# Optimization experiments

Hardware: AMD Instinct MI355X
Metric: run time of the kernel (lower is better)

The kernel has to match this reference:

```python
import jax, jax.numpy as jnp
import numpy as np

EMBED_DIM = 512
NUM_HEADS = 8
HEAD_DIM = EMBED_DIM // NUM_HEADS
SCALE = HEAD_DIM ** -0.5


def setup_inputs() -> dict:
    key = jax.random.key(0)
    k_x, k_qkv, k_o, k_ob = jax.random.split(key, 4)
    x = jax.random.normal(k_x, (2, 2048, EMBED_DIM), dtype=jnp.float32)
    # torch Linear weight is [out, in]; we store transposed [in, out] for x @ W
    w_qkv = jax.random.normal(k_qkv, (EMBED_DIM, 3 * EMBED_DIM), dtype=jnp.float32) * (EMBED_DIM ** -0.5)
    w_o = jax.random.normal(k_o, (EMBED_DIM, EMBED_DIM), dtype=jnp.float32) * (EMBED_DIM ** -0.5)
    b_o = jax.random.normal(k_ob, (EMBED_DIM,), dtype=jnp.float32) * 0.01
    return {"x": x, "w_qkv": w_qkv, "w_o": w_o, "b_o": b_o}


def reference(x, w_qkv, w_o, b_o):
    b, s, e = x.shape
    qkv = x @ w_qkv  # [b, s, 3e]
    q, k, v = jnp.split(qkv, 3, axis=-1)
    # [b, s, e] -> [b, h, s, d]
    def heads(t):
        return t.reshape(b, s, NUM_HEADS, HEAD_DIM).transpose(0, 2, 1, 3)
    q, k, v = heads(q), heads(k), heads(v)
    scores = jnp.einsum("bhqd,bhkd->bhqk", q, k) * SCALE
    attn = jax.nn.softmax(scores, axis=-1)  # dropout = identity in eval
    out = jnp.einsum("bhqk,bhkd->bhqd", attn, v)
    out = out.transpose(0, 2, 1, 3).reshape(b, s, e)
    return out @ w_o + b_o
```

## Files before the change

kernel.cpp:

```cpp
#include <hip/hip_runtime.h>
#include <stdint.h>


typedef __bf16 bf16x8 __attribute__((ext_vector_type(8)));
typedef __bf16 bf16x4 __attribute__((ext_vector_type(4)));
typedef float f32x4 __attribute__((ext_vector_type(4)));
typedef float f32x16 __attribute__((ext_vector_type(16)));

#define MFMA16(a, b, c) __builtin_amdgcn_mfma_f32_16x16x32_bf16((a), (b), (c), 0, 0, 0)
#define MFMA32(a, b, c) __builtin_amdgcn_mfma_f32_32x32x16_bf16((a), (b), (c), 0, 0, 0)
#define QSC 0.18033688011112042f

__device__ __forceinline__ unsigned short f2bf(float f) {
  union { float f; unsigned int u; } v;
  v.f = f;
  unsigned int u = v.u;
  u += 0x7fffu + ((u >> 16) & 1u);
  return (unsigned short)(u >> 16);
}

__device__ __forceinline__ float fast_exp2(float x) {
#if __has_builtin(__builtin_amdgcn_exp2f)
  return __builtin_amdgcn_exp2f(x);
#else
  return exp2f(x);
#endif
}

__device__ __forceinline__ unsigned cvtpk_bf16(float lo, float hi) {
  unsigned r;
  asm("v_cvt_pk_bf16_f32 %0, %1, %2" : "=v"(r) : "v"(lo), "v"(hi));
  return r;
}

__device__ __forceinline__ void gld16(const void* g, void* lds) {
  __builtin_amdgcn_global_load_lds(
      (const __attribute__((address_space(1))) unsigned int*)g,
      (__attribute__((address_space(3))) unsigned int*)lds, 16, 0, 0);
}

__global__ void cvt_kernel(const float* __restrict__ in, unsigned short* __restrict__ out, int n4) {
  int i = blockIdx.x * blockDim.x + threadIdx.x;
  if (i < n4) {
    float4 v = ((const float4*)in)[i];
    ushort4 o;
    o.x = f2bf(v.x); o.y = f2bf(v.y); o.z = f2bf(v.z); o.w = f2bf(v.w);
    ((ushort4*)out)[i] = o;
  }
}

__global__ void tcvt_kernel(const float* __restrict__ in, unsigned short* __restrict__ out, int N) {
  __shared__ unsigned short tile[32][33];
  int tx = threadIdx.x & 31, ty = threadIdx.x >> 5;
  int n0 = blockIdx.x * 32, k0 = blockIdx.y * 32;
#pragma unroll
  for (int i = 0; i < 4; ++i)
    tile[ty + i * 8][tx] = f2bf(in[(k0 + ty + i * 8) * N + n0 + tx]);
  __syncthreads();
#pragma unroll
  for (int i = 0; i < 4; ++i)
    out[(n0 + ty + i * 8) * 512 + k0 + tx] = tile[tx][ty + i * 8];
}

__global__ __launch_bounds__(256, 2) void gemm_qkv(
    const unsigned short* __restrict__ A, const unsigned short* __restrict__ Bt,
    unsigned short* __restrict__ qws, unsigned short* __restrict__ kws,
    unsigned short* __restrict__ vtws) {
  __shared__ __align__(16) unsigned short As[2][128 * 64];
  __shared__ __align__(16) unsigned short Bs[2][128 * 64];
  const int tid = threadIdx.x;
  const int wave = tid >> 6, lane = tid & 63;
  const int quad = lane >> 4, l16 = lane & 15;
  const int waveM = (wave & 1) * 64, waveN = (wave >> 1) * 64;
  const int bm = blockIdx.x, bn = blockIdx.y;

  f32x4 acc[4][4] = {};

  const unsigned short* Ab = A + bm * 128 * 512;
  const unsigned short* Bb = Bt + bn * 128 * 512;

  auto stage = [&](int buf, int k0) {
#pragma unroll
    for (int c = 0; c < 4; ++c) {
      int p = wave * 256 + c * 64 + lane;
      int row = p >> 3;
      int ccl = (p & 7) ^ (row & 7);
      gld16(Ab + row * 512 + k0 + ccl * 8, (char*)(As[buf]) + (wave * 256 + c * 64) * 16);
      gld16(Bb + row * 512 + k0 + ccl * 8, (char*)(Bs[buf]) + (wave * 256 + c * 64) * 16);
    }
  };

  stage(0, 0);
  int cur = 0;
  for (int k0 = 0; k0 < 512; k0 += 64) {
    __syncthreads();
    if (k0 + 64 < 512) stage(cur ^ 1, k0 + 64);
    const unsigned short* Asc = As[cur];
    const unsigned short* Bsc = Bs[cur];
#pragma unroll
    for (int ks = 0; ks < 2; ++ks) {
      bf16x8 af[4], bfr[4];
#pragma unroll
      for (int mb = 0; mb < 4; ++mb) {
        int m = waveM + mb * 16 + l16;
        int cc = (ks * 4 + quad) ^ (m & 7);
        af[mb] = *(const bf16x8*)(Asc + m * 64 + cc * 8);
      }
#pragma unroll
      for (int nb = 0; nb < 4; ++nb) {
        int n = waveN + nb * 16 + l16;
        int cc = (ks * 4 + quad) ^ (n & 7);
        bfr[nb] = *(const bf16x8*)(Bsc + n * 64 + cc * 8);
      }
#pragma unroll
      for (int mb = 0; mb < 4; ++mb)
#pragma unroll
        for (int nb = 0; nb < 4; ++nb)
          acc[mb][nb] = MFMA16(af[mb], bfr[nb], acc[mb][nb]);
    }
    cur ^= 1;
  }

  const int mbase = bm * 128 + waveM;
  const int nbase = bn * 128 + waveN;
  const int region = nbase >> 9;
#pragma unroll
  for (int mb = 0; mb < 4; ++mb) {
    int m0 = mbase + mb * 16 + quad * 4;
    int b = m0 >> 11, s0 = m0 & 2047;
#pragma unroll
    for (int nb = 0; nb < 4; ++nb) {
      int n = nbase + nb * 16 + l16;
      int cix = n & 511;
      int h = cix >> 6, d = cix & 63;
      int bh = b * 8 + h;
      if (region == 0) {
#pragma unroll
        for (int r = 0; r < 4; ++r)
          qws[(bh * 2048 + s0 + r) * 64 + d] = f2bf(acc[mb][nb][r] * QSC);
      } else if (region == 1) {
#pragma unroll
        for (int r = 0; r < 4; ++r)
          kws[(bh * 2048 + s0 + r) * 64 + d] = f2bf(acc[mb][nb][r]);
      } else {
        ushort4 pk;
        pk.x = f2bf(acc[mb][nb][0]);
        pk.y = f2bf(acc[mb][nb][1]);
        pk.z = f2bf(acc[mb][nb][2]);
        pk.w = f2bf(acc[mb][nb][3]);
        *(ushort4*)(vtws + (bh * 64 + d) * 2048 + s0) = pk;
      }
    }
  }
}

__global__ __launch_bounds__(256, 2) void attn_kernel(
    const unsigned short* __restrict__ qws, const unsigned short* __restrict__ kws,
    const unsigned short* __restrict__ vtws, __bf16* __restrict__ opart,
    float* __restrict__ lpart) {
  __shared__ __align__(16) unsigned short Ks[2][64 * 64];
  __shared__ __align__(16) unsigned short Vs[2][64 * 64];
  const int tid = threadIdx.x;
  const int wave = tid >> 6, lane = tid & 63;
  const int l31 = lane & 31, hi = lane >> 5, l7 = lane & 7;
  const int qb = blockIdx.x, bh = blockIdx.y, split = blockIdx.z;

  const unsigned short* Qb = qws + bh * 2048 * 64;
  const unsigned short* Kb = kws + bh * 2048 * 64;
  const unsigned short* Vb = vtws + bh * 64 * 2048;

  const int qbase = qb * 128 + wave * 32;

  bf16x8 qf[4];
#pragma unroll
  for (int kc = 0; kc < 4; ++kc)
    qf[kc] = *(const bf16x8*)(Qb + (qbase + l31) * 64 + kc * 16 + hi * 8);

  float l_lane = 0.f;
  f32x16 oacc[2] = {};

  const int kt0 = split * 16;

  auto stage = [&](int buf, int kt) {
#pragma unroll
    for (int c = 0; c < 2; ++c) {
      int p = wave * 128 + c * 64 + lane;
      int row = p >> 3;
      int ccl = (p & 7) ^ (row & 7);
      gld16(Kb + (kt * 64 + row) * 64 + ccl * 8, (char*)(Ks[buf]) + (wave * 128 + c * 64) * 16);
      gld16(Vb + row * 2048 + kt * 64 + ccl * 8, (char*)(Vs[buf]) + (wave * 128 + c * 64) * 16);
    }
  };

  stage(0, kt0);
  int cur = 0;
  for (int i = 0; i < 16; ++i) {
    __syncthreads();
    if (i + 1 < 16) stage(cur ^ 1, kt0 + i + 1);
    const unsigned short* Kst = Ks[cur];
    const unsigned short* Vst = Vs[cur];

    bf16x8 pa[4];
#pragma unroll
    for (int t = 0; t < 2; ++t) {
      f32x16 sacc = {};
      __builtin_amdgcn_s_setprio(1);
#pragma unroll
      for (int kc = 0; kc < 4; ++kc) {
        bf16x8 kf = *(const bf16x8*)(Kst + (t * 32 + l31) * 64 + (((kc * 2 + hi) ^ l7) * 8));
        sacc = MFMA32(kf, qf[kc], sacc);
      }
      __builtin_amdgcn_s_setprio(0);
      float p[16];
#pragma unroll
      for (int r = 0; r < 16; ++r) p[r] = fast_exp2(sacc[r]);
      float ls = 0.f;
#pragma unroll
      for (int r = 0; r < 16; r += 4) ls += ((p[r] + p[r + 1]) + (p[r + 2] + p[r + 3]));
      l_lane += ls;
#pragma unroll
      for (int kcl = 0; kcl < 2; ++kcl) {
        unsigned c0 = cvtpk_bf16(p[8 * kcl + 0], p[8 * kcl + 1]);
        unsigned c1 = cvtpk_bf16(p[8 * kcl + 2], p[8 * kcl + 3]);
        unsigned c2 = cvtpk_bf16(p[8 * kcl + 4], p[8 * kcl + 5]);
        unsigned c3 = cvtpk_bf16(p[8 * kcl + 6], p[8 * kcl + 7]);
        asm("v_permlane32_swap_b32 %0, %1" : "+v"(c0), "+v"(c2));
        asm("v_permlane32_swap_b32 %0, %1" : "+v"(c1), "+v"(c3));
        union { unsigned u[4]; bf16x8 v; } pk;
        pk.u[0] = c0; pk.u[1] = c1; pk.u[2] = c2; pk.u[3] = c3;
        pa[t * 2 + kcl] = pk.v;
      }
    }

    __builtin_amdgcn_s_setprio(1);
#pragma unroll
    for (int kc2 = 0; kc2 < 4; ++kc2) {
#pragma unroll
      for (int dh = 0; dh < 2; ++dh) {
        bf16x8 vf = *(const bf16x8*)(Vst + (dh * 32 + l31) * 64 + (((kc2 * 2 + hi) ^ l7) * 8));
        oacc[dh] = MFMA32(pa[kc2], vf, oacc[dh]);
      }
    }
    __builtin_amdgcn_s_setprio(0);
    cur ^= 1;
  }

  const long ob = (long)(split * 16 + bh) * 2048;
#pragma unroll
  for (int dh = 0; dh < 2; ++dh)
#pragma unroll
    for (int r = 0; r < 16; ++r) {
      int ql = (r & 3) + 8 * (r >> 2) + 4 * hi;
      opart[(ob + qbase + ql) * 64 + dh * 32 + l31] = (__bf16)oacc[dh][r];
    }
  l_lane += __shfl_xor(l_lane, 32);
  if (hi == 0) lpart[ob + qbase + l31] = l_lane;
}

__global__ void combine_kernel(const __bf16* __restrict__ opart, const float* __restrict__ lpart,
                               unsigned short* __restrict__ ows) {
  int idx = blockIdx.x * 256 + threadIdx.x;
  int dg = idx & 15;
  int q = (idx >> 4) & 2047;
  int bh = idx >> 15;
  bf16x4 o0 = *(const bf16x4*)(opart + ((long)bh * 2048 + q) * 64 + dg * 4);
  bf16x4 o1 = *(const bf16x4*)(opart + ((long)(16 + bh) * 2048 + q) * 64 + dg * 4);
  float inv = 1.0f / (lpart[bh * 2048 + q] + lpart[16 * 2048 + bh * 2048 + q]);
  bf16x4 o;
#pragma unroll
  for (int i = 0; i < 4; ++i) o[i] = (__bf16)(((float)o0[i] + (float)o1[i]) * inv);
  int b = bh >> 3, h = bh & 7;
  *(bf16x4*)((__bf16*)ows + ((long)(b * 2048 + q)) * 512 + h * 64 + dg * 4) = o;
}

__global__ __launch_bounds__(256, 2) void gemm_out(
    const unsigned short* __restrict__ A, const unsigned short* __restrict__ Bt,
    const float* __restrict__ bias, float* __restrict__ out) {
  __shared__ __align__(16) unsigned short As[2][128 * 64];
  __shared__ __align__(16) unsigned short Bs[2][128 * 64];
  const int tid = threadIdx.x;
  const int wave = tid >> 6, lane = tid & 63;
  const int quad = lane >> 4, l16 = lane & 15;
  const int waveM = (wave & 1) * 64, waveN = (wave >> 1) * 64;
  const int bm = blockIdx.x, bn = blockIdx.y;

  f32x4 acc[4][4] = {};

  const unsigned short* Ab = A + bm * 128 * 512;
  const unsigned short* Bb = Bt + bn * 128 * 512;

  auto stage = [&](int buf, int k0) {
#pragma unroll
    for (int c = 0; c < 4; ++c) {
      int p = wave * 256 + c * 64 + lane;
      int row = p >> 3;
      int ccl = (p & 7) ^ (row & 7);
      gld16(Ab + row * 512 + k0 + ccl * 8, (char*)(As[buf]) + (wave * 256 + c * 64) * 16);
      gld16(Bb + row * 512 + k0 + ccl * 8, (char*)(Bs[buf]) + (wave * 256 + c * 64) * 16);
    }
  };

  stage(0, 0);
  int cur = 0;
  for (int k0 = 0; k0 < 512; k0 += 64) {
    __syncthreads();
    if (k0 + 64 < 512) stage(cur ^ 1, k0 + 64);
    const unsigned short* Asc = As[cur];
    const unsigned short* Bsc = Bs[cur];
#pragma unroll
    for (int ks = 0; ks < 2; ++ks) {
      bf16x8 af[4], bfr[4];
#pragma unroll
      for (int mb = 0; mb < 4; ++mb) {
        int m = waveM + mb * 16 + l16;
        int cc = (ks * 4 + quad) ^ (m & 7);
        af[mb] = *(const bf16x8*)(Asc + m * 64 + cc * 8);
      }
#pragma unroll
      for (int nb = 0; nb < 4; ++nb) {
        int n = waveN + nb * 16 + l16;
        int cc = (ks * 4 + quad) ^ (n & 7);
        bfr[nb] = *(const bf16x8*)(Bsc + n * 64 + cc * 8);
      }
#pragma unroll
      for (int mb = 0; mb < 4; ++mb)
#pragma unroll
        for (int nb = 0; nb < 4; ++nb)
          acc[mb][nb] = MFMA16(af[mb], bfr[nb], acc[mb][nb]);
    }
    cur ^= 1;
  }

  const int mbase = bm * 128 + waveM;
  const int nbase = bn * 128 + waveN;
#pragma unroll
  for (int mb = 0; mb < 4; ++mb) {
#pragma unroll
    for (int nb = 0; nb < 4; ++nb) {
      int n = nbase + nb * 16 + l16;
      float bv = bias[n];
#pragma unroll
      for (int r = 0; r < 4; ++r) {
        int m = mbase + mb * 16 + quad * 4 + r;
        out[m * 512 + n] = acc[mb][nb][r] + bv;
      }
    }
  }
}

extern "C" void kernel_launch(void* const* d_in, const int* in_sizes, int n_in,
                              void* d_out, int out_size, void* d_ws, size_t ws_size,
                              hipStream_t stream) {
  const float* x = (const float*)d_in[0];
  const float* w_qkv = (const float*)d_in[1];
  const float* w_o = (const float*)d_in[2];
  const float* b_o = (const float*)d_in[3];
  float* out = (float*)d_out;

  char* ws = (char*)d_ws;
  unsigned short* woT   = (unsigned short*)(ws + 0);
  unsigned short* qws   = (unsigned short*)(ws + 524288);
  unsigned short* kws   = (unsigned short*)(ws + 4718592);
  unsigned short* vtws  = (unsigned short*)(ws + 8912896);
  unsigned short* ows   = (unsigned short*)(ws + 13107200);
  __bf16*         opart = (__bf16*)(ws + 17301504);
  unsigned short* xb    = (unsigned short*)(ws + 17301504);
  unsigned short* wqkvT = (unsigned short*)(ws + 21495808);
  float*          lpart = (float*)(ws + 25690112);

  cvt_kernel<<<2048, 256, 0, stream>>>(x, xb, 524288);
  tcvt_kernel<<<dim3(48, 16), 256, 0, stream>>>(w_qkv, wqkvT, 1536);
  tcvt_kernel<<<dim3(16, 16), 256, 0, stream>>>(w_o, woT, 512);
  gemm_qkv<<<dim3(32, 12), 256, 0, stream>>>(xb, wqkvT, qws, kws, vtws);
  attn_kernel<<<dim3(16, 16, 2), 256, 0, stream>>>(qws, kws, vtws, opart, lpart);
  combine_kernel<<<2048, 256, 0, stream>>>(opart, lpart, ows);
  gemm_out<<<dim3(32, 4), 256, 0, stream>>>(ows, woT, b_o, out);
}
```

Before: 126.6 us.

## Fuse split-KV combine into output GEMM A-staging and merge prep kernels

Merges the three conversion and transpose kernels into one prep kernel dispatched by block index, which saves two launches. Removes the separate combine kernel: the output projection GEMM now reads both attention partials and their softmax denominators, normalizes them, and writes the bf16 A tile straight into shared memory. The GEMM tile M is halved to 64, giving a 64x4 grid for more blocks. The cost is that A staging becomes synchronous register loads instead of async global-to-LDS copies, and the combine work is repeated for each of the 4 N-blocks.

Measured after the change: 120.0 us. 1.06x faster.

```diff
diff --git a/kernel.cpp b/kernel.cpp
--- a/kernel.cpp
+++ b/kernel.cpp
@@ -39,27 +39,33 @@
       (__attribute__((address_space(3))) unsigned int*)lds, 16, 0, 0);
 }
 
-__global__ void cvt_kernel(const float* __restrict__ in, unsigned short* __restrict__ out, int n4) {
-  int i = blockIdx.x * blockDim.x + threadIdx.x;
-  if (i < n4) {
-    float4 v = ((const float4*)in)[i];
+__global__ void prep_kernel(const float* __restrict__ x, unsigned short* __restrict__ xb,
+                            const float* __restrict__ w_qkv, unsigned short* __restrict__ wqkvT,
+                            const float* __restrict__ w_o, unsigned short* __restrict__ woT) {
+  __shared__ unsigned short tile[32][33];
+  const int bid = blockIdx.x, tid = threadIdx.x;
+  if (bid < 2048) {
+    int i = bid * 256 + tid;
+    float4 v = ((const float4*)x)[i];
     ushort4 o;
     o.x = f2bf(v.x); o.y = f2bf(v.y); o.z = f2bf(v.z); o.w = f2bf(v.w);
-    ((ushort4*)out)[i] = o;
-  }
-}
-
-__global__ void tcvt_kernel(const float* __restrict__ in, unsigned short* __restrict__ out, int N) {
-  __shared__ unsigned short tile[32][33];
-  int tx = threadIdx.x & 31, ty = threadIdx.x >> 5;
-  int n0 = blockIdx.x * 32, k0 = blockIdx.y * 32;
-#pragma unroll
-  for (int i = 0; i < 4; ++i)
-    tile[ty + i * 8][tx] = f2bf(in[(k0 + ty + i * 8) * N + n0 + tx]);
-  __syncthreads();
-#pragma unroll
-  for (int i = 0; i < 4; ++i)
-    out[(n0 + ty + i * 8) * 512 + k0 + tx] = tile[tx][ty + i * 8];
+    ((ushort4*)xb)[i] = o;
+  } else {
+    const float* in;
+    unsigned short* out;
+    int N, bx, by;
+    if (bid < 2816) { int t = bid - 2048; bx = t % 48; by = t / 48; in = w_qkv; out = wqkvT; N = 1536; }
+    else            { int t = bid - 2816; bx = t & 15; by = t >> 4;  in = w_o;  out = woT;  N = 512;  }
+    int tx = tid & 31, ty = tid >> 5;
+    int n0 = bx * 32, k0 = by * 32;
+#pragma unroll
+    for (int i = 0; i < 4; ++i)
+      tile[ty + i * 8][tx] = f2bf(in[(k0 + ty + i * 8) * N + n0 + tx]);
+    __syncthreads();
+#pragma unroll
+    for (int i = 0; i < 4; ++i)
+      out[(n0 + ty + i * 8) * 512 + k0 + tx] = tile[tx][ty + i * 8];
+  }
 }
 
 __global__ __launch_bounds__(256, 2) void gemm_qkv(
@@ -257,61 +263,64 @@
   if (hi == 0) lpart[ob + qbase + l31] = l_lane;
 }
 
-__global__ void combine_kernel(const __bf16* __restrict__ opart, const float* __restrict__ lpart,
-                               unsigned short* __restrict__ ows) {
-  int idx = blockIdx.x * 256 + threadIdx.x;
-  int dg = idx & 15;
-  int q = (idx >> 4) & 2047;
-  int bh = idx >> 15;
-  bf16x4 o0 = *(const bf16x4*)(opart + ((long)bh * 2048 + q) * 64 + dg * 4);
-  bf16x4 o1 = *(const bf16x4*)(opart + ((long)(16 + bh) * 2048 + q) * 64 + dg * 4);
-  float inv = 1.0f / (lpart[bh * 2048 + q] + lpart[16 * 2048 + bh * 2048 + q]);
-  bf16x4 o;
-#pragma unroll
-  for (int i = 0; i < 4; ++i) o[i] = (__bf16)(((float)o0[i] + (float)o1[i]) * inv);
-  int b = bh >> 3, h = bh & 7;
-  *(bf16x4*)((__bf16*)ows + ((long)(b * 2048 + q)) * 512 + h * 64 + dg * 4) = o;
-}
-
 __global__ __launch_bounds__(256, 2) void gemm_out(
-    const unsigned short* __restrict__ A, const unsigned short* __restrict__ Bt,
-    const float* __restrict__ bias, float* __restrict__ out) {
-  __shared__ __align__(16) unsigned short As[2][128 * 64];
+    const __bf16* __restrict__ opart, const float* __restrict__ lpart,
+    const unsigned short* __restrict__ Bt, const float* __restrict__ bias,
+    float* __restrict__ out) {
+  __shared__ __align__(16) unsigned short As[2][64 * 64];
   __shared__ __align__(16) unsigned short Bs[2][128 * 64];
   const int tid = threadIdx.x;
   const int wave = tid >> 6, lane = tid & 63;
   const int quad = lane >> 4, l16 = lane & 15;
-  const int waveM = (wave & 1) * 64, waveN = (wave >> 1) * 64;
+  const int waveM = (wave & 1) * 32, waveN = (wave >> 1) * 64;
   const int bm = blockIdx.x, bn = blockIdx.y;
 
-  f32x4 acc[4][4] = {};
-
-  const unsigned short* Ab = A + bm * 128 * 512;
+  f32x4 acc[2][4] = {};
+
   const unsigned short* Bb = Bt + bn * 128 * 512;
 
-  auto stage = [&](int buf, int k0) {
+  auto stageB = [&](int buf, int k0) {
 #pragma unroll
     for (int c = 0; c < 4; ++c) {
       int p = wave * 256 + c * 64 + lane;
       int row = p >> 3;
       int ccl = (p & 7) ^ (row & 7);
-      gld16(Ab + row * 512 + k0 + ccl * 8, (char*)(As[buf]) + (wave * 256 + c * 64) * 16);
       gld16(Bb + row * 512 + k0 + ccl * 8, (char*)(Bs[buf]) + (wave * 256 + c * 64) * 16);
     }
   };
-
-  stage(0, 0);
+  auto stageA = [&](int buf, int k0) {
+    const int h = k0 >> 6;
+#pragma unroll
+    for (int c = 0; c < 2; ++c) {
+      int p = wave * 128 + c * 64 + lane;
+      int row = p >> 3;
+      int ccl = (p & 7) ^ (row & 7);
+      int m = bm * 64 + row;
+      int q = m & 2047, b = m >> 11;
+      int bh = b * 8 + h;
+      bf16x8 o0 = *(const bf16x8*)(opart + ((long)bh * 2048 + q) * 64 + ccl * 8);
+      bf16x8 o1 = *(const bf16x8*)(opart + ((long)(16 + bh) * 2048 + q) * 64 + ccl * 8);
+      float inv = 1.0f / (lpart[bh * 2048 + q] + lpart[(16 + bh) * 2048 + q]);
+      bf16x8 v;
+#pragma unroll
+      for (int j = 0; j < 8; ++j) v[j] = (__bf16)(((float)o0[j] + (float)o1[j]) * inv);
+      *(bf16x8*)((char*)(As[buf]) + p * 16) = v;
+    }
+  };
+
+  stageB(0, 0);
+  stageA(0, 0);
   int cur = 0;
   for (int k0 = 0; k0 < 512; k0 += 64) {
     __syncthreads();
-    if (k0 + 64 < 512) stage(cur ^ 1, k0 + 64);
+    if (k0 + 64 < 512) { stageB(cur ^ 1, k0 + 64); stageA(cur ^ 1, k0 + 64); }
     const unsigned short* Asc = As[cur];
     const unsigned short* Bsc = Bs[cur];
 #pragma unroll
     for (int ks = 0; ks < 2; ++ks) {
-      bf16x8 af[4], bfr[4];
-#pragma unroll
-      for (int mb = 0; mb < 4; ++mb) {
+      bf16x8 af[2], bfr[4];
+#pragma unroll
+      for (int mb = 0; mb < 2; ++mb) {
         int m = waveM + mb * 16 + l16;
         int cc = (ks * 4 + quad) ^ (m & 7);
         af[mb] = *(const bf16x8*)(Asc + m * 64 + cc * 8);
@@ -323,7 +332,7 @@
         bfr[nb] = *(const bf16x8*)(Bsc + n * 64 + cc * 8);
       }
 #pragma unroll
-      for (int mb = 0; mb < 4; ++mb)
+      for (int mb = 0; mb < 2; ++mb)
 #pragma unroll
         for (int nb = 0; nb < 4; ++nb)
           acc[mb][nb] = MFMA16(af[mb], bfr[nb], acc[mb][nb]);
@@ -331,10 +340,10 @@
     cur ^= 1;
   }
 
-  const int mbase = bm * 128 + waveM;
+  const int mbase = bm * 64 + waveM;
   const int nbase = bn * 128 + waveN;
 #pragma unroll
-  for (int mb = 0; mb < 4; ++mb) {
+  for (int mb = 0; mb < 2; ++mb) {
 #pragma unroll
     for (int nb = 0; nb < 4; ++nb) {
       int n = nbase + nb * 16 + l16;
@@ -362,17 +371,13 @@
   unsigned short* qws   = (unsigned short*)(ws + 524288);
   unsigned short* kws   = (unsigned short*)(ws + 4718592);
   unsigned short* vtws  = (unsigned short*)(ws + 8912896);
-  unsigned short* ows   = (unsigned short*)(ws + 13107200);
   __bf16*         opart = (__bf16*)(ws + 17301504);
   unsigned short* xb    = (unsigned short*)(ws + 17301504);
   unsigned short* wqkvT = (unsigned short*)(ws + 21495808);
   float*          lpart = (float*)(ws + 25690112);
 
-  cvt_kernel<<<2048, 256, 0, stream>>>(x, xb, 524288);
-  tcvt_kernel<<<dim3(48, 16), 256, 0, stream>>>(w_qkv, wqkvT, 1536);
-  tcvt_kernel<<<dim3(16, 16), 256, 0, stream>>>(w_o, woT, 512);
+  prep_kernel<<<3072, 256, 0, stream>>>(x, xb, w_qkv, wqkvT, w_o, woT);
   gemm_qkv<<<dim3(32, 12), 256, 0, stream>>>(xb, wqkvT, qws, kws, vtws);
   attn_kernel<<<dim3(16, 16, 2), 256, 0, stream>>>(qws, kws, vtws, opart, lpart);
-  combine_kernel<<<2048, 256, 0, stream>>>(opart, lpart, ows);
-  gemm_out<<<dim3(32, 4), 256, 0, stream>>>(ows, woT, b_o, out);
-}
+  gemm_out<<<dim3(64, 4), 256, 0, stream>>>(opart, lpart, woT, b_o, out);
+}
```
